# Kernel optimization log

Hardware: AMD Instinct MI355X
Metric: run time of the kernel (lower is better)

## Reference

```python
import jax, jax.numpy as jnp
import numpy as np

EPS = 1e-7  # keras.backend.epsilon()
ROUTINGS = 3
N_IN, D_IN = 2048, 16
CAPS_N, CAPS_DIM = 64, 32
BATCH = 32


def squash(x, axis=-1):
    s2 = jnp.sum(jnp.square(x), axis=axis, keepdims=True) + EPS
    return (jnp.sqrt(s2) / (1.0 + s2)) * x


def setup_inputs() -> dict:
    key = jax.random.key(0)
    kx, kw = jax.random.split(key)
    x = jax.random.normal(kx, (BATCH, N_IN, D_IN), dtype=jnp.float32)
    # glorot_uniform for W: fan_in = caps_dim_in, fan_out = caps_dim_out (per matmul tile)
    limit = np.sqrt(6.0 / (D_IN + CAPS_DIM))
    W = jax.random.uniform(kw, (N_IN, CAPS_N, CAPS_DIM, D_IN), minval=-limit, maxval=limit, dtype=jnp.float32)
    return {"x": x, "W": W}


def reference(x, W):
    # caps_predicted (u_hat): W[i,k] @ x[b,i] -> [B, n_in, caps_n, caps_dim]
    u_hat = jnp.einsum('ikdl,bil->bikd', W, x)
    # routing logits, broadcast over batch like the original [1, n_in, caps_n, 1, 1]
    b = jnp.zeros((1, N_IN, CAPS_N), dtype=x.dtype)
    v = None
    for r in range(ROUTINGS):
        c = jax.nn.softmax(b, axis=2)                      # [*, n_in, caps_n]
        s = jnp.sum(c[..., None] * u_hat, axis=1)          # [B, caps_n, caps_dim]
        v = squash(s, axis=-1)                             # [B, caps_n, caps_dim]
        if r < ROUTINGS - 1:
            # agreement = u_hat^T . v  -> [B, n_in, caps_n]
            agreement = jnp.einsum('bikd,bkd->bik', u_hat, v)
            b = b + agreement
    return v
```

## Files before the change

### kernel.cpp

```cpp
#include <hip/hip_runtime.h>
#include <hip/hip_fp16.h>

#define BB 32
#define NI 2048
#define NK 64
#define KD 2048
#define NL 16
#define IT 8
#define NTC (NI/IT)
#define RCH 32
#define NRC (NI/RCH)
#define EPSF 1e-7f

typedef _Float16 h2 __attribute__((ext_vector_type(2)));
union UH2  { unsigned u; h2 h; };
union U4H8 { uint4 u4; h2 h[4]; };

static __device__ __forceinline__ float dot2f(h2 a, h2 b, float c) {
#if __has_builtin(__builtin_amdgcn_fdot2)
  return __builtin_amdgcn_fdot2(a, b, c, false);
#else
  return c + (float)a[0] * (float)b[0] + (float)a[1] * (float)b[1];
#endif
}

static __device__ __forceinline__ h2 pack2(float x, float y) {
  h2 r; r[0] = (_Float16)x; r[1] = (_Float16)y; return r;
}

__global__ __launch_bounds__(512, 4) void k_conv(const float* __restrict__ x,
                                                 const float* __restrict__ W,
                                                 __half* __restrict__ uhat,
                                                 __half* __restrict__ part) {
  const int blk = blockIdx.x, half = blockIdx.y, t = threadIdx.x;
  const int i0 = blk * IT;
  const int c0 = half * 1024 + 2 * t;
  __shared__ h2 xs[IT][BB][8];
  for (int q = t; q < IT * BB * 8; q += 512) {
    const int l2 = q & 7, b = (q >> 3) & 31, ii = q >> 8;
    const float2 f = *(const float2*)&x[((size_t)b * NI + (i0 + ii)) * NL + 2 * l2];
    xs[ii][b][l2] = pack2(f.x, f.y);
  }
  __syncthreads();

  float sacc0[BB], sacc1[BB];
  #pragma unroll
  for (int b = 0; b < BB; ++b) { sacc0[b] = 0.f; sacc1[b] = 0.f; }

  for (int ii = 0; ii < IT; ++ii) {
    const float* Wp = W + ((size_t)(i0 + ii) * KD + c0) * NL;
    h2 w0[8], w1[8];
    #pragma unroll
    for (int q = 0; q < 4; ++q) {
      const float4 f = *(const float4*)(Wp + 4 * q);
      w0[2 * q] = pack2(f.x, f.y); w0[2 * q + 1] = pack2(f.z, f.w);
    }
    #pragma unroll
    for (int q = 0; q < 4; ++q) {
      const float4 f = *(const float4*)(Wp + NL + 4 * q);
      w1[2 * q] = pack2(f.x, f.y); w1[2 * q + 1] = pack2(f.z, f.w);
    }
    #pragma unroll
    for (int b = 0; b < BB; ++b) {
      U4H8 ux0, ux1;
      ux0.u4 = *(const uint4*)&xs[ii][b][0];
      ux1.u4 = *(const uint4*)&xs[ii][b][4];
      float u0 = 0.f, u1 = 0.f;
      #pragma unroll
      for (int j = 0; j < 4; ++j) {
        u0 = dot2f(w0[j], ux0.h[j], u0); u0 = dot2f(w0[4 + j], ux1.h[j], u0);
        u1 = dot2f(w1[j], ux0.h[j], u1); u1 = dot2f(w1[4 + j], ux1.h[j], u1);
      }
      UH2 p; p.h = pack2(u0, u1);
      *(unsigned*)&uhat[((size_t)b * NI + (i0 + ii)) * KD + c0] = p.u;
      sacc0[b] += u0; sacc1[b] += u1;
    }
  }
  #pragma unroll
  for (int b = 0; b < BB; ++b) {
    UH2 p; p.h = pack2(sacc0[b] * (1.f / 64.f), sacc1[b] * (1.f / 64.f));
    *(unsigned*)&part[((size_t)b * NTC + blk) * KD + c0] = p.u;
  }
}

__global__ __launch_bounds__(256) void k_route(const __half* __restrict__ uhat,
                                               const float* __restrict__ vin,
                                               __half* __restrict__ part) {
  const int ch = blockIdx.x, b = blockIdx.y, t = threadIdx.x;
  const int lane = t & 63, wv = t >> 6;
  __shared__ float ssum[2][4];
  float vr[8];
  *(float4*)&vr[0] = *(const float4*)&vin[(size_t)b * KD + 8 * t];
  *(float4*)&vr[4] = *(const float4*)&vin[(size_t)b * KD + 8 * t + 4];
  float sacc[8];
  #pragma unroll
  for (int j = 0; j < 8; ++j) sacc[j] = 0.f;

  const __half* up = uhat + ((size_t)b * NI + (size_t)ch * RCH) * KD + 8 * t;
  U4H8 cur; cur.u4 = *(const uint4*)up;
  for (int il = 0; il < RCH; ++il) {
    U4H8 nxt;
    if (il + 1 < RCH) nxt.u4 = *(const uint4*)(up + (size_t)(il + 1) * KD);
    float uf[8];
    #pragma unroll
    for (int j = 0; j < 4; ++j) {
      uf[2 * j] = (float)cur.h[j][0];
      uf[2 * j + 1] = (float)cur.h[j][1];
    }
    float ag = 0.f;
    #pragma unroll
    for (int j = 0; j < 8; ++j) ag += uf[j] * vr[j];
    ag += __shfl_xor(ag, 1);
    ag += __shfl_xor(ag, 2);
    const float e = __expf(ag);
    float s = e;
    s += __shfl_xor(s, 4);  s += __shfl_xor(s, 8);
    s += __shfl_xor(s, 16); s += __shfl_xor(s, 32);
    if (lane == 0) ssum[il & 1][wv] = s;
    __syncthreads();
    const float stot = ssum[il & 1][0] + ssum[il & 1][1] +
                       ssum[il & 1][2] + ssum[il & 1][3];
    const float c = e / stot;
    #pragma unroll
    for (int j = 0; j < 8; ++j) sacc[j] += c * uf[j];
    cur = nxt;
  }
  U4H8 o;
  o.h[0] = pack2(sacc[0], sacc[1]); o.h[1] = pack2(sacc[2], sacc[3]);
  o.h[2] = pack2(sacc[4], sacc[5]); o.h[3] = pack2(sacc[6], sacc[7]);
  *(uint4*)&part[((size_t)b * NRC + ch) * KD + 8 * t] = o.u4;
}

__global__ __launch_bounds__(256) void k_reduce(const __half* __restrict__ part,
                                                int nch,
                                                const float* __restrict__ vprev,
                                                float* __restrict__ vout) {
  const int g = blockIdx.x, b = blockIdx.y, t = threadIdx.x;
  const int p = g * 256 + t;
  const h2* pp = (const h2*)part;
  const size_t base = (size_t)b * nch * (KD / 2) + p;
  float s0 = 0.f, s1 = 0.f;
  for (int ch = 0; ch < nch; ++ch) {
    const h2 v = pp[base + (size_t)ch * (KD / 2)];
    s0 += (float)v[0]; s1 += (float)v[1];
  }
  float sq = s0 * s0 + s1 * s1;
  sq += __shfl_xor(sq, 1); sq += __shfl_xor(sq, 2);
  sq += __shfl_xor(sq, 4); sq += __shfl_xor(sq, 8);
  sq += EPSF;
  const float sc = sqrtf(sq) / (1.f + sq);
  float r0 = s0 * sc, r1 = s1 * sc;
  if (vprev != nullptr) {
    r0 += vprev[(size_t)b * KD + 2 * p];
    r1 += vprev[(size_t)b * KD + 2 * p + 1];
  }
  *(float2*)&vout[(size_t)b * KD + 2 * p] = make_float2(r0, r1);
}

extern "C" void kernel_launch(void* const* d_in, const int* in_sizes, int n_in,
                              void* d_out, int out_size, void* d_ws, size_t ws_size,
                              hipStream_t stream) {
  const float* x = (const float*)d_in[0];
  const float* W = (const float*)d_in[1];
  float* out = (float*)d_out;
  char* ws = (char*)d_ws;
  __half* uhat  = (__half*)ws;
  __half* part0 = (__half*)(ws + 268435456ull);
  __half* partR = (__half*)(ws + 268435456ull + 33554432ull);
  float*  vA    = (float*)(ws + 268435456ull + 33554432ull + 8388608ull);
  float*  vB    = vA + (size_t)BB * KD;

  k_conv<<<dim3(NTC, 2), 512, 0, stream>>>(x, W, uhat, part0);
  k_reduce<<<dim3(4, BB), 256, 0, stream>>>(part0, NTC, nullptr, vA);
  k_route<<<dim3(NRC, BB), 256, 0, stream>>>(uhat, vA, partR);
  k_reduce<<<dim3(4, BB), 256, 0, stream>>>(partR, NRC, vA, vB);
  k_route<<<dim3(NRC, BB), 256, 0, stream>>>(uhat, vB, partR);
  k_reduce<<<dim3(4, BB), 256, 0, stream>>>(partR, NRC, nullptr, out);
}
```

Measured before the change: 344.0 us.

## Compute u_hat in fp32 FMA with one output column per thread

The projection kernel drops the packed fp16 dot2 path and computes each u_hat element with fp32 FMAs. Each thread now owns one output column instead of two, and the grid doubles in y to cover all columns. x is staged in shared memory as fp32 and W is loaded without conversion. This removes the conversion and packing work and raises the number of blocks. The trade-offs are 2-byte fp16 stores that are less coalesced, roughly twice the scalar FMA work, and a lower occupancy hint.

```diff
diff --git a/kernel.cpp b/kernel.cpp
--- a/kernel.cpp
+++ b/kernel.cpp
@@ -16,71 +16,52 @@
 union UH2  { unsigned u; h2 h; };
 union U4H8 { uint4 u4; h2 h[4]; };
 
-static __device__ __forceinline__ float dot2f(h2 a, h2 b, float c) {
-#if __has_builtin(__builtin_amdgcn_fdot2)
-  return __builtin_amdgcn_fdot2(a, b, c, false);
-#else
-  return c + (float)a[0] * (float)b[0] + (float)a[1] * (float)b[1];
-#endif
-}
-
 static __device__ __forceinline__ h2 pack2(float x, float y) {
   h2 r; r[0] = (_Float16)x; r[1] = (_Float16)y; return r;
 }
 
-__global__ __launch_bounds__(512, 4) void k_conv(const float* __restrict__ x,
+__global__ __launch_bounds__(512, 2) void k_conv(const float* __restrict__ x,
                                                  const float* __restrict__ W,
                                                  __half* __restrict__ uhat,
                                                  __half* __restrict__ part) {
-  const int blk = blockIdx.x, half = blockIdx.y, t = threadIdx.x;
+  const int blk = blockIdx.x, quad = blockIdx.y, t = threadIdx.x;
   const int i0 = blk * IT;
-  const int c0 = half * 1024 + 2 * t;
-  __shared__ h2 xs[IT][BB][8];
-  for (int q = t; q < IT * BB * 8; q += 512) {
-    const int l2 = q & 7, b = (q >> 3) & 31, ii = q >> 8;
-    const float2 f = *(const float2*)&x[((size_t)b * NI + (i0 + ii)) * NL + 2 * l2];
-    xs[ii][b][l2] = pack2(f.x, f.y);
+  const int c0 = quad * 512 + t;
+  __shared__ float xs[IT][BB][NL];
+  for (int q = t; q < IT * BB * 4; q += 512) {
+    const int l4 = q & 3, b = (q >> 2) & 31, ii = q >> 7;
+    *(float4*)&xs[ii][b][4 * l4] =
+        *(const float4*)&x[((size_t)b * NI + (i0 + ii)) * NL + 4 * l4];
   }
   __syncthreads();
 
-  float sacc0[BB], sacc1[BB];
+  float sacc[BB];
   #pragma unroll
-  for (int b = 0; b < BB; ++b) { sacc0[b] = 0.f; sacc1[b] = 0.f; }
+  for (int b = 0; b < BB; ++b) sacc[b] = 0.f;
 
   for (int ii = 0; ii < IT; ++ii) {
     const float* Wp = W + ((size_t)(i0 + ii) * KD + c0) * NL;
-    h2 w0[8], w1[8];
+    float w[NL];
     #pragma unroll
-    for (int q = 0; q < 4; ++q) {
-      const float4 f = *(const float4*)(Wp + 4 * q);
-      w0[2 * q] = pack2(f.x, f.y); w0[2 * q + 1] = pack2(f.z, f.w);
-    }
-    #pragma unroll
-    for (int q = 0; q < 4; ++q) {
-      const float4 f = *(const float4*)(Wp + NL + 4 * q);
-      w1[2 * q] = pack2(f.x, f.y); w1[2 * q + 1] = pack2(f.z, f.w);
-    }
+    for (int q = 0; q < 4; ++q)
+      *(float4*)&w[4 * q] = *(const float4*)(Wp + 4 * q);
     #pragma unroll
     for (int b = 0; b < BB; ++b) {
-      U4H8 ux0, ux1;
-      ux0.u4 = *(const uint4*)&xs[ii][b][0];
-      ux1.u4 = *(const uint4*)&xs[ii][b][4];
-      float u0 = 0.f, u1 = 0.f;
-      #pragma unroll
-      for (int j = 0; j < 4; ++j) {
-        u0 = dot2f(w0[j], ux0.h[j], u0); u0 = dot2f(w0[4 + j], ux1.h[j], u0);
-        u1 = dot2f(w1[j], ux0.h[j], u1); u1 = dot2f(w1[4 + j], ux1.h[j], u1);
-      }
-      UH2 p; p.h = pack2(u0, u1);
-      *(unsigned*)&uhat[((size_t)b * NI + (i0 + ii)) * KD + c0] = p.u;
-      sacc0[b] += u0; sacc1[b] += u1;
+      float4 x0 = *(const float4*)&xs[ii][b][0];
+      float4 x1 = *(const float4*)&xs[ii][b][4];
+      float4 x2 = *(const float4*)&xs[ii][b][8];
+      float4 x3 = *(const float4*)&xs[ii][b][12];
+      float u = w[0] * x0.x + w[1] * x0.y + w[2] * x0.z + w[3] * x0.w
+              + w[4] * x1.x + w[5] * x1.y + w[6] * x1.z + w[7] * x1.w
+              + w[8] * x2.x + w[9] * x2.y + w[10] * x2.z + w[11] * x2.w
+              + w[12] * x3.x + w[13] * x3.y + w[14] * x3.z + w[15] * x3.w;
+      uhat[((size_t)b * NI + (i0 + ii)) * KD + c0] = (__half)u;
+      sacc[b] += u;
     }
   }
   #pragma unroll
-  for (int b = 0; b < BB; ++b) {
-    UH2 p; p.h = pack2(sacc0[b] * (1.f / 64.f), sacc1[b] * (1.f / 64.f));
-    *(unsigned*)&part[((size_t)b * NTC + blk) * KD + c0] = p.u;
-  }
+  for (int b = 0; b < BB; ++b)
+    part[((size_t)b * NTC + blk) * KD + c0] = (__half)(sacc[b] * (1.f / 64.f));
 }
 
 __global__ __launch_bounds__(256) void k_route(const __half* __restrict__ uhat,
@@ -170,7 +151,7 @@
   float*  vA    = (float*)(ws + 268435456ull + 33554432ull + 8388608ull);
   float*  vB    = vA + (size_t)BB * KD;
 
-  k_conv<<<dim3(NTC, 2), 512, 0, stream>>>(x, W, uhat, part0);
+  k_conv<<<dim3(NTC, 4), 512, 0, stream>>>(x, W, uhat, part0);
   k_reduce<<<dim3(4, BB), 256, 0, stream>>>(part0, NTC, nullptr, vA);
   k_route<<<dim3(NRC, BB), 256, 0, stream>>>(uhat, vA, partR);
   k_reduce<<<dim3(4, BB), 256, 0, stream>>>(partR, NRC, vA, vB);
```

Result: slower. 443.0 us (+28.8%).

## Use MFMA for u_hat projection and remap routing to one wave per input capsule

Applied to the files above, without the earlier changes.

The conv kernel now computes u_hat with 16x16x32 f16 MFMA instructions over batch and capsule-cell tiles instead of scalar dot2 loops. It zero-pads half of the K dimension and writes uhat with scattered 2-byte stores. The routing kernel now gives each wave one input capsule, so every lane holds a full 32-dim capsule. That turns the softmax into a single wave-level shuffle reduction and removes the per-step __syncthreads. The cost is more partial outputs for the reduce kernel to sum, and the uhat stores in conv are less coalesced.

```diff
diff --git a/kernel.cpp b/kernel.cpp
--- a/kernel.cpp
+++ b/kernel.cpp
@@ -4,16 +4,21 @@
 #define BB 32
 #define NI 2048
 #define NK 64
+#define ND 32
 #define KD 2048
 #define NL 16
-#define IT 8
-#define NTC (NI/IT)
-#define RCH 32
-#define NRC (NI/RCH)
+#define ITC 8
+#define NTC (NI/ITC)
+#define RIB 64
+#define NRC (NI/RIB)
+#define RIW (RIB/4)
+#define NPR (NRC*4)
 #define EPSF 1e-7f
 
+typedef _Float16 f16;
+typedef __attribute__((ext_vector_type(8))) _Float16 f16x8;
+typedef __attribute__((ext_vector_type(4))) float f32x4;
 typedef _Float16 h2 __attribute__((ext_vector_type(2)));
-union UH2  { unsigned u; h2 h; };
 union U4H8 { uint4 u4; h2 h[4]; };
 
 static __device__ __forceinline__ float dot2f(h2 a, h2 b, float c) {
@@ -28,58 +33,53 @@
   h2 r; r[0] = (_Float16)x; r[1] = (_Float16)y; return r;
 }
 
-__global__ __launch_bounds__(512, 4) void k_conv(const float* __restrict__ x,
-                                                 const float* __restrict__ W,
-                                                 __half* __restrict__ uhat,
-                                                 __half* __restrict__ part) {
-  const int blk = blockIdx.x, half = blockIdx.y, t = threadIdx.x;
-  const int i0 = blk * IT;
-  const int c0 = half * 1024 + 2 * t;
-  __shared__ h2 xs[IT][BB][8];
-  for (int q = t; q < IT * BB * 8; q += 512) {
-    const int l2 = q & 7, b = (q >> 3) & 31, ii = q >> 8;
-    const float2 f = *(const float2*)&x[((size_t)b * NI + (i0 + ii)) * NL + 2 * l2];
-    xs[ii][b][l2] = pack2(f.x, f.y);
-  }
-  __syncthreads();
+__global__ __launch_bounds__(256) void k_conv(const float* __restrict__ x,
+                                              const float* __restrict__ W,
+                                              __half* __restrict__ uhat,
+                                              __half* __restrict__ part) {
+  const int blk = blockIdx.x, cg = blockIdx.y, t = threadIdx.x;
+  const int wv = t >> 6, lane = t & 63;
+  const int n = lane & 15, g = lane >> 4;
+  const int i0 = blk * ITC;
 
-  float sacc0[BB], sacc1[BB];
+  f16x8 A[2][ITC];
   #pragma unroll
-  for (int b = 0; b < BB; ++b) { sacc0[b] = 0.f; sacc1[b] = 0.f; }
+  for (int h = 0; h < 2; ++h)
+    #pragma unroll
+    for (int ii = 0; ii < ITC; ++ii) {
+      const f32x4 xv = *(const f32x4*)&x[((size_t)(h * 16 + n) * NI + (i0 + ii)) * NL + 4 * g];
+      f16x8 a;
+      a[0] = (f16)xv[0]; a[1] = (f16)xv[1]; a[2] = (f16)xv[2]; a[3] = (f16)xv[3];
+      a[4] = a[0]; a[5] = a[1]; a[6] = a[2]; a[7] = a[3];
+      A[h][ii] = a;
+    }
 
-  for (int ii = 0; ii < IT; ++ii) {
-    const float* Wp = W + ((size_t)(i0 + ii) * KD + c0) * NL;
-    h2 w0[8], w1[8];
-    #pragma unroll
-    for (int q = 0; q < 4; ++q) {
-      const float4 f = *(const float4*)(Wp + 4 * q);
-      w0[2 * q] = pack2(f.x, f.y); w0[2 * q + 1] = pack2(f.z, f.w);
+  for (int nt = 0; nt < 8; ++nt) {
+    const int cell0 = (cg * 32 + wv * 8 + nt) * 16;
+    float pacc0[4] = {0.f, 0.f, 0.f, 0.f};
+    float pacc1[4] = {0.f, 0.f, 0.f, 0.f};
+    for (int ii = 0; ii < ITC; ++ii) {
+      const f32x4 wv4 = *(const f32x4*)&W[((size_t)(i0 + ii) * KD + cell0 + n) * NL + 4 * g];
+      f16x8 bf = {0, 0, 0, 0, 0, 0, 0, 0};
+      bf[0] = (f16)wv4[0]; bf[1] = (f16)wv4[1]; bf[2] = (f16)wv4[2]; bf[3] = (f16)wv4[3];
+      const f32x4 z = {0.f, 0.f, 0.f, 0.f};
+      const f32x4 D0 = __builtin_amdgcn_mfma_f32_16x16x32_f16(A[0][ii], bf, z, 0, 0, 0);
+      const f32x4 D1 = __builtin_amdgcn_mfma_f32_16x16x32_f16(A[1][ii], bf, z, 0, 0, 0);
+      #pragma unroll
+      for (int j = 0; j < 4; ++j) {
+        const int b0 = 4 * g + j;
+        uhat[((size_t)b0 * NI + (i0 + ii)) * KD + cell0 + n] = (__half)D0[j];
+        uhat[((size_t)(b0 + 16) * NI + (i0 + ii)) * KD + cell0 + n] = (__half)D1[j];
+        pacc0[j] += D0[j];
+        pacc1[j] += D1[j];
+      }
     }
     #pragma unroll
-    for (int q = 0; q < 4; ++q) {
-      const float4 f = *(const float4*)(Wp + NL + 4 * q);
-      w1[2 * q] = pack2(f.x, f.y); w1[2 * q + 1] = pack2(f.z, f.w);
+    for (int j = 0; j < 4; ++j) {
+      const int b0 = 4 * g + j;
+      part[((size_t)b0 * NTC + blk) * KD + cell0 + n] = (__half)(pacc0[j] * (1.f / 64.f));
+      part[((size_t)(b0 + 16) * NTC + blk) * KD + cell0 + n] = (__half)(pacc1[j] * (1.f / 64.f));
     }
-    #pragma unroll
-    for (int b = 0; b < BB; ++b) {
-      U4H8 ux0, ux1;
-      ux0.u4 = *(const uint4*)&xs[ii][b][0];
-      ux1.u4 = *(const uint4*)&xs[ii][b][4];
-      float u0 = 0.f, u1 = 0.f;
-      #pragma unroll
-      for (int j = 0; j < 4; ++j) {
-        u0 = dot2f(w0[j], ux0.h[j], u0); u0 = dot2f(w0[4 + j], ux1.h[j], u0);
-        u1 = dot2f(w1[j], ux0.h[j], u1); u1 = dot2f(w1[4 + j], ux1.h[j], u1);
-      }
-      UH2 p; p.h = pack2(u0, u1);
-      *(unsigned*)&uhat[((size_t)b * NI + (i0 + ii)) * KD + c0] = p.u;
-      sacc0[b] += u0; sacc1[b] += u1;
-    }
-  }
-  #pragma unroll
-  for (int b = 0; b < BB; ++b) {
-    UH2 p; p.h = pack2(sacc0[b] * (1.f / 64.f), sacc1[b] * (1.f / 64.f));
-    *(unsigned*)&part[((size_t)b * NTC + blk) * KD + c0] = p.u;
   }
 }
 
@@ -87,48 +87,68 @@
                                                const float* __restrict__ vin,
                                                __half* __restrict__ part) {
   const int ch = blockIdx.x, b = blockIdx.y, t = threadIdx.x;
-  const int lane = t & 63, wv = t >> 6;
-  __shared__ float ssum[2][4];
-  float vr[8];
-  *(float4*)&vr[0] = *(const float4*)&vin[(size_t)b * KD + 8 * t];
-  *(float4*)&vr[4] = *(const float4*)&vin[(size_t)b * KD + 8 * t + 4];
-  float sacc[8];
+  const int wv = t >> 6, lane = t & 63;
+
+  h2 vh[16];
   #pragma unroll
-  for (int j = 0; j < 8; ++j) sacc[j] = 0.f;
+  for (int q = 0; q < 4; ++q) {
+    const f32x4 v0 = *(const f32x4*)&vin[(size_t)b * KD + lane * ND + 8 * q];
+    const f32x4 v1 = *(const f32x4*)&vin[(size_t)b * KD + lane * ND + 8 * q + 4];
+    vh[4 * q + 0] = pack2(v0[0], v0[1]); vh[4 * q + 1] = pack2(v0[2], v0[3]);
+    vh[4 * q + 2] = pack2(v1[0], v1[1]); vh[4 * q + 3] = pack2(v1[2], v1[3]);
+  }
 
-  const __half* up = uhat + ((size_t)b * NI + (size_t)ch * RCH) * KD + 8 * t;
-  U4H8 cur; cur.u4 = *(const uint4*)up;
-  for (int il = 0; il < RCH; ++il) {
-    U4H8 nxt;
-    if (il + 1 < RCH) nxt.u4 = *(const uint4*)(up + (size_t)(il + 1) * KD);
-    float uf[8];
-    #pragma unroll
-    for (int j = 0; j < 4; ++j) {
-      uf[2 * j] = (float)cur.h[j][0];
-      uf[2 * j + 1] = (float)cur.h[j][1];
+  float sacc[32];
+  #pragma unroll
+  for (int d = 0; d < 32; ++d) sacc[d] = 0.f;
+
+  const __half* ub = uhat + (size_t)b * NI * KD + lane * ND;
+  const int ibase = ch * RIB + wv;
+  U4H8 cur[4];
+  #pragma unroll
+  for (int q = 0; q < 4; ++q)
+    cur[q].u4 = *(const uint4*)(ub + (size_t)ibase * KD + 8 * q);
+
+  for (int il = 0; il < RIW; ++il) {
+    U4H8 nxt[4];
+    if (il + 1 < RIW) {
+      const size_t ioff = (size_t)(ibase + 4 * (il + 1)) * KD;
+      #pragma unroll
+      for (int q = 0; q < 4; ++q)
+        nxt[q].u4 = *(const uint4*)(ub + ioff + 8 * q);
     }
     float ag = 0.f;
     #pragma unroll
-    for (int j = 0; j < 8; ++j) ag += uf[j] * vr[j];
-    ag += __shfl_xor(ag, 1);
-    ag += __shfl_xor(ag, 2);
+    for (int q = 0; q < 4; ++q)
+      #pragma unroll
+      for (int j = 0; j < 4; ++j)
+        ag = dot2f(cur[q].h[j], vh[4 * q + j], ag);
     const float e = __expf(ag);
     float s = e;
-    s += __shfl_xor(s, 4);  s += __shfl_xor(s, 8);
-    s += __shfl_xor(s, 16); s += __shfl_xor(s, 32);
-    if (lane == 0) ssum[il & 1][wv] = s;
-    __syncthreads();
-    const float stot = ssum[il & 1][0] + ssum[il & 1][1] +
-                       ssum[il & 1][2] + ssum[il & 1][3];
-    const float c = e / stot;
+    s += __shfl_xor(s, 1);  s += __shfl_xor(s, 2);  s += __shfl_xor(s, 4);
+    s += __shfl_xor(s, 8);  s += __shfl_xor(s, 16); s += __shfl_xor(s, 32);
+    const float c = e / s;
     #pragma unroll
-    for (int j = 0; j < 8; ++j) sacc[j] += c * uf[j];
-    cur = nxt;
+    for (int q = 0; q < 4; ++q)
+      #pragma unroll
+      for (int j = 0; j < 4; ++j) {
+        sacc[8 * q + 2 * j]     += c * (float)cur[q].h[j][0];
+        sacc[8 * q + 2 * j + 1] += c * (float)cur[q].h[j][1];
+      }
+    #pragma unroll
+    for (int q = 0; q < 4; ++q) cur[q] = nxt[q];
   }
-  U4H8 o;
-  o.h[0] = pack2(sacc[0], sacc[1]); o.h[1] = pack2(sacc[2], sacc[3]);
-  o.h[2] = pack2(sacc[4], sacc[5]); o.h[3] = pack2(sacc[6], sacc[7]);
-  *(uint4*)&part[((size_t)b * NRC + ch) * KD + 8 * t] = o.u4;
+
+  U4H8 o[4];
+  #pragma unroll
+  for (int q = 0; q < 4; ++q)
+    #pragma unroll
+    for (int j = 0; j < 4; ++j)
+      o[q].h[j] = pack2(sacc[8 * q + 2 * j], sacc[8 * q + 2 * j + 1]);
+  __half* pp = part + (((size_t)b * NRC + ch) * 4 + wv) * KD + lane * ND;
+  #pragma unroll
+  for (int q = 0; q < 4; ++q)
+    *(uint4*)(pp + 8 * q) = o[q].u4;
 }
 
 __global__ __launch_bounds__(256) void k_reduce(const __half* __restrict__ part,
@@ -166,14 +186,14 @@
   char* ws = (char*)d_ws;
   __half* uhat  = (__half*)ws;
   __half* part0 = (__half*)(ws + 268435456ull);
-  __half* partR = (__half*)(ws + 268435456ull + 33554432ull);
-  float*  vA    = (float*)(ws + 268435456ull + 33554432ull + 8388608ull);
+  __half* partR = part0;
+  float*  vA    = (float*)(ws + 268435456ull + 33554432ull);
   float*  vB    = vA + (size_t)BB * KD;
 
-  k_conv<<<dim3(NTC, 2), 512, 0, stream>>>(x, W, uhat, part0);
+  k_conv<<<dim3(NTC, 4), 256, 0, stream>>>(x, W, uhat, part0);
   k_reduce<<<dim3(4, BB), 256, 0, stream>>>(part0, NTC, nullptr, vA);
   k_route<<<dim3(NRC, BB), 256, 0, stream>>>(uhat, vA, partR);
-  k_reduce<<<dim3(4, BB), 256, 0, stream>>>(partR, NRC, vA, vB);
+  k_reduce<<<dim3(4, BB), 256, 0, stream>>>(partR, NPR, vA, vB);
   k_route<<<dim3(NRC, BB), 256, 0, stream>>>(uhat, vB, partR);
-  k_reduce<<<dim3(4, BB), 256, 0, stream>>>(partR, NRC, nullptr, out);
+  k_reduce<<<dim3(4, BB), 256, 0, stream>>>(partR, NPR, nullptr, out);
 }
```

Result: slower. 569.4 us (+65.5%).
